# Kernel tuning notes

Measured on AMD Instinct MI355X. Metric: run time of the kernel, lower is better.

The kernel has to match this reference:

```python
import jax, jax.numpy as jnp
import numpy as np

HID = 5120
H_DEV = 16          # 128 heads / 8 devices
NOPE = 128
ROPE = 64
VDIM = 128
QH = NOPE + ROPE    # 192
Q_LORA = 1536
KV_LORA = 512
EPS = 1e-6
SCALE_DEV = 1.0 / 8.0
ROPE_BASE = 10000.0


def rmsnorm(x, w):
    var = jnp.mean(x * x, axis=-1, keepdims=True)
    return x * jax.lax.rsqrt(var + EPS) * w


def apply_rope(x, pos):
    # DeepSeek-V2: interleaved->blocked reorder, then rotate-half RoPE.
    d = x.shape[-1]
    x = jnp.concatenate([x[..., 0::2], x[..., 1::2]], axis=-1)
    inv = 1.0 / (ROPE_BASE ** (jnp.arange(0, d, 2, dtype=jnp.float32) / d))  # [d/2]
    ang = pos[:, None, :, None].astype(jnp.float32) * inv                     # [b,1,s,d/2]
    cos = jnp.concatenate([jnp.cos(ang), jnp.cos(ang)], axis=-1)
    sin = jnp.concatenate([jnp.sin(ang), jnp.sin(ang)], axis=-1)
    x1, x2 = x[..., : d // 2], x[..., d // 2:]
    return x * cos + jnp.concatenate([-x2, x1], axis=-1) * sin


def setup_inputs() -> dict:
    key = jax.random.key(0)
    ks = jax.random.split(key, 16)
    b, s, past = 1, 2048, 2048
    w = lambda k, shape: (jax.random.normal(k, shape, jnp.float32) * 0.02)
    return {
        "hidden_states": jax.random.normal(ks[0], (b, s, HID), jnp.float32),
        "position_ids": jnp.arange(b * s, dtype=jnp.int32).reshape(b, s),
        "attention_mask": jnp.zeros((b, 1, s, past + s), jnp.float32),
        "past_k": jax.random.normal(ks[1], (b, H_DEV, past, QH), jnp.float32),
        "past_v": jax.random.normal(ks[2], (b, H_DEV, past, VDIM), jnp.float32),
        "w_in_ln": jnp.ones((HID,), jnp.float32),
        "w_qa": w(ks[3], (Q_LORA, HID)),
        "w_qa_ln": jnp.ones((Q_LORA,), jnp.float32),
        "w_qb": w(ks[4], (H_DEV * QH, Q_LORA)),
        "w_kva": w(ks[5], (KV_LORA + ROPE, HID)),
        "w_kva_ln": jnp.ones((KV_LORA,), jnp.float32),
        "w_kvb": w(ks[6], (H_DEV * (NOPE + VDIM), KV_LORA)),
        "w_o": w(ks[7], (HID, H_DEV * VDIM)),
    }


def reference(hidden_states, position_ids, attention_mask, past_k, past_v,
              w_in_ln, w_qa, w_qa_ln, w_qb, w_kva, w_kva_ln, w_kvb, w_o):
    b, s, _ = hidden_states.shape
    residual = hidden_states * SCALE_DEV
    x = rmsnorm(hidden_states, w_in_ln)

    # MLA query: low-rank down, RMSNorm, up to per-device heads
    q = rmsnorm(x @ w_qa.T, w_qa_ln) @ w_qb.T                       # [b,s,H*QH]
    q = q.reshape(b, s, H_DEV, QH).transpose(0, 2, 1, 3)            # [b,H,s,QH]
    q_nope, q_pe = q[..., :NOPE], q[..., NOPE:]

    # MLA key/value: joint compressed kv + shared rope key
    ckv = x @ w_kva.T                                                # [b,s,KV_LORA+ROPE]
    c_kv, k_pe = ckv[..., :KV_LORA], ckv[..., KV_LORA:]
    kv = rmsnorm(c_kv, w_kva_ln) @ w_kvb.T                           # [b,s,H*(NOPE+V)]
    kv = kv.reshape(b, s, H_DEV, NOPE + VDIM).transpose(0, 2, 1, 3)  # [b,H,s,NOPE+V]
    k_nope, v = kv[..., :NOPE], kv[..., NOPE:]
    k_pe = k_pe.reshape(b, 1, s, ROPE)

    q_pe = apply_rope(q_pe, position_ids)
    k_pe = apply_rope(k_pe, position_ids)

    q = jnp.concatenate([q_nope, q_pe], axis=-1)                     # [b,H,s,QH]
    k = jnp.concatenate([k_nope, jnp.broadcast_to(k_pe, (b, H_DEV, s, ROPE))], axis=-1)

    # KV-cache concat -> present kv
    k = jnp.concatenate([past_k, k], axis=2)                         # [b,H,s_kv,QH]
    v = jnp.concatenate([past_v, v], axis=2)                         # [b,H,s_kv,V]

    scores = jnp.einsum('bhqd,bhkd->bhqk', q, k) * (QH ** -0.5) + attention_mask
    attn = jax.nn.softmax(scores, axis=-1)
    ctx = jnp.einsum('bhqk,bhkd->bhqd', attn, v)                     # [b,H,s,V]
    ctx = ctx.transpose(0, 2, 1, 3).reshape(b, s, H_DEV * VDIM)

    out = residual + ctx @ w_o.T
    return out.astype(jnp.float32), k.astype(jnp.float32), v.astype(jnp.float32)
```

## Files before the change

### kernel.cpp

```cpp
#include <hip/hip_runtime.h>
#include <cstdint>

typedef unsigned short ushort_t;
typedef __attribute__((ext_vector_type(8))) short short8;
typedef __attribute__((ext_vector_type(4))) float floatx4;

#define HID    5120
#define NHEAD  16
#define NOPE   128
#define ROPE_D 64
#define VDIM   128
#define QHD    192
#define QLORA  1536
#define KVLORA 512
#define SEQ    2048
#define PAST   2048
#define TOTK   4096
#define EPS_RMS 1e-6f
#define SCALE_DEV 0.125f
#define LOG2E 1.4426950408889634f
#define ATT_SCALE 0.07216878364870322f
#define LOG2_10000 13.287712379549449f

__device__ __forceinline__ float bf2f(ushort_t u) {
  unsigned int x = ((unsigned int)u) << 16;
  return __builtin_bit_cast(float, x);
}
__device__ __forceinline__ ushort_t f2bf(float f) {
  unsigned int u = __builtin_bit_cast(unsigned int, f);
  unsigned int r = u + 0x7fffu + ((u >> 16) & 1u);
  return (ushort_t)(r >> 16);
}
__device__ __forceinline__ void unpack8(uint4 c, float* f) {
  const ushort_t* p = (const ushort_t*)&c;
#pragma unroll
  for (int i = 0; i < 8; ++i) f[i] = bf2f(p[i]);
}
__device__ __forceinline__ uint4 pack8(const float* f) {
  uint4 c;
  ushort_t* p = (ushort_t*)&c;
#pragma unroll
  for (int i = 0; i < 8; ++i) p[i] = f2bf(f[i]);
  return c;
}

__global__ void cvt_kernel(const float* __restrict__ src, ushort_t* __restrict__ dst)
{
  long i = ((long)blockIdx.x * 256 + threadIdx.x) * 8;
  float f[8];
  *(float4*)(f)     = *(const float4*)(src + i);
  *(float4*)(f + 4) = *(const float4*)(src + i + 4);
  *(uint4*)(dst + i) = pack8(f);
}

#define GLDT 40
__global__ __launch_bounds__(256, 2) void gemm_bt(
    const ushort_t* __restrict__ A, const ushort_t* __restrict__ B,
    ushort_t* __restrict__ Cb, float* __restrict__ Cf,
    const float* __restrict__ resid, float resid_scale,
    int M, int N, int K)
{
  __shared__ __align__(16) ushort_t As[128 * GLDT];
  __shared__ __align__(16) ushort_t Bs[128 * GLDT];
  int t = threadIdx.x;
  int lane = t & 63, wave = t >> 6;
  int wm = wave >> 1, wn = wave & 1;
  int lrow = lane & 15, quad = lane >> 4;
  long bm = (long)blockIdx.y * 128;
  long bn = (long)blockIdx.x * 128;

  int r0 = t >> 2, cc = t & 3;
  int r1 = r0 + 64;
  const ushort_t* a0 = A + (bm + r0) * (long)K + cc * 8;
  const ushort_t* a1 = A + (bm + r1) * (long)K + cc * 8;
  long nb0 = bn + r0; if (nb0 > N - 1) nb0 = N - 1;
  long nb1 = bn + r1; if (nb1 > N - 1) nb1 = N - 1;
  const ushort_t* b0 = B + nb0 * (long)K + cc * 8;
  const ushort_t* b1 = B + nb1 * (long)K + cc * 8;

  floatx4 acc[4][4];
#pragma unroll
  for (int i = 0; i < 4; ++i)
#pragma unroll
    for (int j = 0; j < 4; ++j) acc[i][j] = (floatx4)0.f;

  uint4 pa0 = *(const uint4*)a0;
  uint4 pa1 = *(const uint4*)a1;
  uint4 pb0 = *(const uint4*)b0;
  uint4 pb1 = *(const uint4*)b1;

  int nk = K >> 5;
  for (int kt = 0; kt < nk; ++kt) {
    *(uint4*)&As[r0 * GLDT + cc * 8] = pa0;
    *(uint4*)&As[r1 * GLDT + cc * 8] = pa1;
    *(uint4*)&Bs[r0 * GLDT + cc * 8] = pb0;
    *(uint4*)&Bs[r1 * GLDT + cc * 8] = pb1;
    __syncthreads();
    if (kt + 1 < nk) {
      int off = (kt + 1) << 5;
      pa0 = *(const uint4*)(a0 + off);
      pa1 = *(const uint4*)(a1 + off);
      pb0 = *(const uint4*)(b0 + off);
      pb1 = *(const uint4*)(b1 + off);
    }
    short8 af[4], bfr[4];
#pragma unroll
    for (int mt = 0; mt < 4; ++mt)
      af[mt] = *(const short8*)&As[(wm * 64 + mt * 16 + lrow) * GLDT + quad * 8];
#pragma unroll
    for (int nt = 0; nt < 4; ++nt)
      bfr[nt] = *(const short8*)&Bs[(wn * 64 + nt * 16 + lrow) * GLDT + quad * 8];
#pragma unroll
    for (int mt = 0; mt < 4; ++mt)
#pragma unroll
      for (int nt = 0; nt < 4; ++nt)
        acc[mt][nt] = __builtin_amdgcn_mfma_f32_16x16x32_bf16(af[mt], bfr[nt], acc[mt][nt], 0, 0, 0);
    __syncthreads();
  }

#pragma unroll
  for (int mt = 0; mt < 4; ++mt) {
    long grow = bm + wm * 64 + mt * 16 + quad * 4;
#pragma unroll
    for (int nt = 0; nt < 4; ++nt) {
      long gcol = bn + wn * 64 + nt * 16 + lrow;
      if (gcol < N) {
#pragma unroll
        for (int r2 = 0; r2 < 4; ++r2) {
          long row = grow + r2;
          float v = acc[mt][nt][r2];
          if (Cf) {
            if (resid) v += resid_scale * resid[row * (long)N + gcol];
            Cf[row * (long)N + gcol] = v;
          } else {
            Cb[row * (long)N + gcol] = f2bf(v);
          }
        }
      }
    }
  }
}

__global__ void rms_in_kernel(const float* __restrict__ x,
                              const float* __restrict__ w,
                              ushort_t* __restrict__ out)
{
  int row = blockIdx.x, t = threadIdx.x;
  const float* xr = x + (long)row * HID + t * 16;
  float v[16];
#pragma unroll
  for (int i = 0; i < 4; ++i) *(float4*)(v + i * 4) = *(const float4*)(xr + i * 4);
  float ss = 0.f;
#pragma unroll
  for (int i = 0; i < 16; ++i) ss += v[i] * v[i];
#pragma unroll
  for (int o = 1; o < 64; o <<= 1) ss += __shfl_xor(ss, o);
  __shared__ float red[5];
  if ((t & 63) == 0) red[t >> 6] = ss;
  __syncthreads();
  float tot = red[0] + red[1] + red[2] + red[3] + red[4];
  float sc = rsqrtf(tot / (float)HID + EPS_RMS);
  float wv[16];
#pragma unroll
  for (int i = 0; i < 4; ++i) *(float4*)(wv + i * 4) = *(const float4*)(w + t * 16 + i * 4);
#pragma unroll
  for (int i = 0; i < 16; ++i) v[i] *= sc * wv[i];
  ushort_t* o = out + (long)row * HID + t * 16;
  *(uint4*)o       = pack8(v);
  *(uint4*)(o + 8) = pack8(v + 8);
}

__global__ void rms_qa_kernel(const ushort_t* __restrict__ x,
                              const float* __restrict__ w,
                              ushort_t* __restrict__ out)
{
  int row = blockIdx.x, t = threadIdx.x;
  const ushort_t* xr = x + (long)row * QLORA;
  float v[8];
  unpack8(*(const uint4*)(xr + t * 8), v);
  float ss = 0.f;
#pragma unroll
  for (int i = 0; i < 8; ++i) ss += v[i] * v[i];
#pragma unroll
  for (int o = 1; o < 64; o <<= 1) ss += __shfl_xor(ss, o);
  __shared__ float red[3];
  if ((t & 63) == 0) red[t >> 6] = ss;
  __syncthreads();
  float tot = red[0] + red[1] + red[2];
  float sc = rsqrtf(tot / (float)QLORA + EPS_RMS);
  float wv[8];
  *(float4*)(wv)     = *(const float4*)(w + t * 8);
  *(float4*)(wv + 4) = *(const float4*)(w + t * 8 + 4);
#pragma unroll
  for (int i = 0; i < 8; ++i) v[i] *= sc * wv[i];
  *(uint4*)(out + (long)row * QLORA + t * 8) = pack8(v);
}

__global__ void rms_ckv_rope(const ushort_t* __restrict__ ckv_raw,
                             const float* __restrict__ w,
                             const int* __restrict__ pos_ids,
                             ushort_t* __restrict__ ckv_n,
                             ushort_t* __restrict__ kpe,
                             float* __restrict__ k_out)
{
  int row = blockIdx.x, t = threadIdx.x;
  const ushort_t* xr = ckv_raw + (long)row * 576;
  float v[8];
  unpack8(*(const uint4*)(xr + t * 8), v);
  float ss = 0.f;
#pragma unroll
  for (int i = 0; i < 8; ++i) ss += v[i] * v[i];
#pragma unroll
  for (int o = 1; o < 64; o <<= 1) ss += __shfl_xor(ss, o);
  float sc = rsqrtf(ss / (float)KVLORA + EPS_RMS);
  float wv[8];
  *(float4*)(wv)     = *(const float4*)(w + t * 8);
  *(float4*)(wv + 4) = *(const float4*)(w + t * 8 + 4);
  float ov[8];
#pragma unroll
  for (int i = 0; i < 8; ++i) ov[i] = v[i] * sc * wv[i];
  *(uint4*)(ckv_n + (long)row * KVLORA + t * 8) = pack8(ov);

  if (t < 32) {
    float e  = bf2f(xr[512 + 2 * t]);
    float od = bf2f(xr[512 + 2 * t + 1]);
    float p = (float)pos_ids[row];
    float inv = __builtin_exp2f(-((float)t / 32.f) * LOG2_10000);
    float ang = p * inv, sn, cs;
    sincosf(ang, &sn, &cs);
    float r1 = e * cs - od * sn;
    float r2 = od * cs + e * sn;
    kpe[(long)row * 64 + t]      = f2bf(r1);
    kpe[(long)row * 64 + 32 + t] = f2bf(r2);
#pragma unroll
    for (int h = 0; h < NHEAD; ++h) {
      float* kr = k_out + ((long)h * TOTK + PAST + row) * QHD + NOPE;
      kr[t] = r1;
      kr[32 + t] = r2;
    }
  }
}

__global__ void qpost_kernel(const ushort_t* __restrict__ q_raw,
                             const int* __restrict__ pos_ids,
                             ushort_t* __restrict__ q_bf)
{
  int row = blockIdx.x, t = threadIdx.x;
  const ushort_t* qr = q_raw + (long)row * 3072;
  ushort_t* qo = q_bf + (long)row * 3072;
  {
    int hh = t >> 4, c = t & 15;
    float v[8];
    unpack8(*(const uint4*)(qr + hh * QHD + c * 8), v);
#pragma unroll
    for (int i = 0; i < 8; ++i) v[i] *= ATT_SCALE;
    *(uint4*)(qo + hh * QHD + c * 8) = pack8(v);
  }
  float p = (float)pos_ids[row];
#pragma unroll
  for (int it = 0; it < 2; ++it) {
    int slot = t + it * 256;
    int hh = slot >> 5, i = slot & 31;
    float e  = bf2f(qr[hh * QHD + NOPE + 2 * i]);
    float od = bf2f(qr[hh * QHD + NOPE + 2 * i + 1]);
    float inv = __builtin_exp2f(-((float)i / 32.f) * LOG2_10000);
    float ang = p * inv, sn, cs;
    sincosf(ang, &sn, &cs);
    qo[hh * QHD + NOPE + i]      = f2bf((e * cs - od * sn) * ATT_SCALE);
    qo[hh * QHD + NOPE + 32 + i] = f2bf((od * cs + e * sn) * ATT_SCALE);
  }
}

__global__ void kvpost_kernel(const ushort_t* __restrict__ kv_raw,
                              float* __restrict__ k_out,
                              float* __restrict__ v_out)
{
  int row = blockIdx.x, t = threadIdx.x;
  const ushort_t* kr = kv_raw + (long)row * 4096;
#pragma unroll
  for (int it = 0; it < 2; ++it) {
    int c = t + it * 256;
    int hh = c >> 5, cc = c & 31;
    float v[8];
    unpack8(*(const uint4*)(kr + c * 8), v);
    float* dst;
    if (cc < 16) dst = k_out + ((long)hh * TOTK + PAST + row) * QHD + cc * 8;
    else         dst = v_out + ((long)hh * TOTK + PAST + row) * VDIM + (cc - 16) * 8;
    floatx4 f0 = {v[0], v[1], v[2], v[3]};
    floatx4 f1 = {v[4], v[5], v[6], v[7]};
    *(floatx4*)dst = f0;
    *(floatx4*)(dst + 4) = f1;
  }
}

__global__ void past_kernel(const float* __restrict__ past_k,
                            const float* __restrict__ past_v,
                            float* __restrict__ k_out,
                            float* __restrict__ v_out)
{
  long c = (long)blockIdx.x * 256 + threadIdx.x;
  if (c < 1572864) {
    float4 v = *(const float4*)(past_k + c * 4);
    long hh = c / 98304, rem = c % 98304;
    long s = rem / 48, cc = rem % 48;
    *(float4*)(k_out + (hh * (long)TOTK + s) * QHD + cc * 4) = v;
  } else {
    long c2 = c - 1572864;
    float4 v = *(const float4*)(past_v + c2 * 4);
    long hh = c2 / 65536, rem = c2 % 65536;
    long s = rem / 32, cc = rem % 32;
    *(float4*)(v_out + (hh * (long)TOTK + s) * VDIM + cc * 4) = v;
  }
}

__global__ void buildK_kernel(const float* __restrict__ past_k,
                              const ushort_t* __restrict__ kv_raw,
                              const ushort_t* __restrict__ kpe,
                              ushort_t* __restrict__ Kc)
{
  long g = (long)blockIdx.x * 256 + threadIdx.x;
  int ko = (int)(g & 63);
  long r = g >> 6;
  int cc = (int)(r % 24);
  long r2 = r / 24;
  int kt = (int)(r2 & 63);
  int hh = (int)(r2 >> 6);
  int key = kt * 64 + ko;
  uint4 val;
  if (key < PAST) {
    const float* src = past_k + ((long)hh * PAST + key) * QHD + cc * 8;
    float f[8];
    *(float4*)(f)     = *(const float4*)src;
    *(float4*)(f + 4) = *(const float4*)(src + 4);
    val = pack8(f);
  } else {
    int s = key - PAST;
    int d0 = cc * 8;
    if (d0 < NOPE) val = *(const uint4*)(kv_raw + (long)s * 4096 + hh * 256 + d0);
    else           val = *(const uint4*)(kpe + (long)s * 64 + (d0 - NOPE));
  }
  *(uint4*)(Kc + g * 8) = val;
}

__global__ void buildV_kernel(const float* __restrict__ past_v,
                              const ushort_t* __restrict__ kv_raw,
                              ushort_t* __restrict__ Vc)
{
  long tid = (long)blockIdx.x * 256 + threadIdx.x;
  int vd = (int)(tid & 127);
  long r = tid >> 7;
  int kchunk = (int)(r & 7);
  long r2 = r >> 3;
  int kt = (int)(r2 & 63);
  int hh = (int)(r2 >> 6);
  int key0 = kt * 64 + kchunk * 8;
  __align__(16) ushort_t tmp[8];
  if (key0 < PAST) {
#pragma unroll
    for (int j = 0; j < 8; ++j)
      tmp[j] = f2bf(past_v[((long)hh * PAST + key0 + j) * VDIM + vd]);
  } else {
    int s = key0 - PAST;
#pragma unroll
    for (int j = 0; j < 8; ++j)
      tmp[j] = kv_raw[(long)(s + j) * 4096 + hh * 256 + NOPE + vd];
  }
  *(uint4*)(Vc + ((((long)hh * 64 + kt) * 128 + vd) * 9 + kchunk) * 8) = *(uint4*)tmp;
}

__global__ __launch_bounds__(256, 2) void attn_kernel(
    const ushort_t* __restrict__ qb,
    const ushort_t* __restrict__ Kc,
    const ushort_t* __restrict__ Vc,
    const float* __restrict__ attn_mask,
    ushort_t* __restrict__ ctx)
{
  __shared__ __align__(16) ushort_t KtL[1536 * 8];
  __shared__ __align__(16) ushort_t VtL[1152 * 8];
  __shared__ __align__(16) ushort_t Pl[4 * 16 * 72];

  int t = threadIdx.x, lane = t & 63, wave = t >> 6;
  int lrow = lane & 15, quad = lane >> 4;
  int h = blockIdx.y;
  int q0 = blockIdx.x * 64;
  int qrow_a = q0 + wave * 16 + lrow;
  int qrow_c = q0 + wave * 16 + quad * 4;

  short8 aq[6];
  const ushort_t* qp = qb + ((long)qrow_a * 16 + h) * QHD + quad * 8;
#pragma unroll
  for (int kc = 0; kc < 6; ++kc) aq[kc] = *(const short8*)(qp + kc * 32);

  float m_r[4], l_r[4];
  floatx4 cacc[8];
#pragma unroll
  for (int r = 0; r < 4; ++r) { m_r[r] = -1e30f; l_r[r] = 0.f; }
#pragma unroll
  for (int v = 0; v < 8; ++v) cacc[v] = (floatx4)0.f;

  const ushort_t* Kbase = Kc + (long)h * 64 * 1536 * 8;
  const ushort_t* Vbase = Vc + (long)h * 64 * 1152 * 8;

  for (int kt2 = 0; kt2 < 64; ++kt2) {
    const ushort_t* ks = Kbase + (long)kt2 * 1536 * 8;
#pragma unroll
    for (int i = 0; i < 6; ++i) {
      int s = i * 256 + t;
      *(uint4*)&KtL[s * 8] = *(const uint4*)(ks + (long)s * 8);
    }
    const ushort_t* vs = Vbase + (long)kt2 * 1152 * 8;
#pragma unroll
    for (int i = 0; i < 5; ++i) {
      int s = i * 256 + t;
      if (s < 1152) *(uint4*)&VtL[s * 8] = *(const uint4*)(vs + (long)s * 8);
    }
    __syncthreads();

    floatx4 sacc[4];
#pragma unroll
    for (int nt = 0; nt < 4; ++nt) sacc[nt] = (floatx4)0.f;
#pragma unroll
    for (int kc = 0; kc < 6; ++kc) {
#pragma unroll
      for (int nt = 0; nt < 4; ++nt) {
        short8 bk = *(const short8*)&KtL[(((kc * 4 + quad) * 64) + nt * 16 + lrow) * 8];
        sacc[nt] = __builtin_amdgcn_mfma_f32_16x16x32_bf16(aq[kc], bk, sacc[nt], 0, 0, 0);
      }
    }

    int kbase = kt2 * 64;
    float sv[4][4];
#pragma unroll
    for (int nt = 0; nt < 4; ++nt)
#pragma unroll
      for (int r = 0; r < 4; ++r)
        sv[nt][r] = sacc[nt][r] +
                    attn_mask[(long)(qrow_c + r) * TOTK + kbase + nt * 16 + lrow];

    float alpha[4];
#pragma unroll
    for (int r = 0; r < 4; ++r) {
      float mx = fmaxf(fmaxf(sv[0][r], sv[1][r]), fmaxf(sv[2][r], sv[3][r]));
      mx = fmaxf(mx, __shfl_xor(mx, 1));
      mx = fmaxf(mx, __shfl_xor(mx, 2));
      mx = fmaxf(mx, __shfl_xor(mx, 4));
      mx = fmaxf(mx, __shfl_xor(mx, 8));
      float mn = fmaxf(m_r[r], mx);
      alpha[r] = __builtin_exp2f((m_r[r] - mn) * LOG2E);
      m_r[r] = mn;
      float rs = 0.f;
#pragma unroll
      for (int nt = 0; nt < 4; ++nt) {
        float p = __builtin_exp2f((sv[nt][r] - mn) * LOG2E);
        sv[nt][r] = p;
        rs += p;
      }
      rs += __shfl_xor(rs, 1);
      rs += __shfl_xor(rs, 2);
      rs += __shfl_xor(rs, 4);
      rs += __shfl_xor(rs, 8);
      l_r[r] = l_r[r] * alpha[r] + rs;
    }
#pragma unroll
    for (int v = 0; v < 8; ++v) {
      floatx4 c = cacc[v];
      c[0] *= alpha[0]; c[1] *= alpha[1]; c[2] *= alpha[2]; c[3] *= alpha[3];
      cacc[v] = c;
    }

    ushort_t* pw = &Pl[wave * 16 * 72];
#pragma unroll
    for (int nt = 0; nt < 4; ++nt)
#pragma unroll
      for (int r = 0; r < 4; ++r)
        pw[(quad * 4 + r) * 72 + nt * 16 + lrow] = f2bf(sv[nt][r]);
    __syncthreads();

    const ushort_t* pr = &Pl[wave * 16 * 72];
    short8 ap[2];
#pragma unroll
    for (int kc = 0; kc < 2; ++kc)
      ap[kc] = *(const short8*)(pr + lrow * 72 + kc * 32 + quad * 8);
#pragma unroll
    for (int kc = 0; kc < 2; ++kc) {
#pragma unroll
      for (int v = 0; v < 8; ++v) {
        short8 bv = *(const short8*)&VtL[(((v * 16 + lrow) * 9) + kc * 4 + quad) * 8];
        cacc[v] = __builtin_amdgcn_mfma_f32_16x16x32_bf16(ap[kc], bv, cacc[v], 0, 0, 0);
      }
    }
    __syncthreads();
  }

#pragma unroll
  for (int v = 0; v < 8; ++v)
#pragma unroll
    for (int r = 0; r < 4; ++r) {
      float o = cacc[v][r] / l_r[r];
      ctx[(long)(qrow_c + r) * 2048 + h * 128 + v * 16 + lrow] = f2bf(o);
    }
}

extern "C" void kernel_launch(void* const* d_in, const int* in_sizes, int n_in,
                              void* d_out, int out_size, void* d_ws, size_t ws_size,
                              hipStream_t stream)
{
  const float* hidden   = (const float*)d_in[0];
  const int*   pos      = (const int*)d_in[1];
  const float* mask     = (const float*)d_in[2];
  const float* past_k   = (const float*)d_in[3];
  const float* past_v   = (const float*)d_in[4];
  const float* w_in_ln  = (const float*)d_in[5];
  const float* w_qa     = (const float*)d_in[6];
  const float* w_qa_ln  = (const float*)d_in[7];
  const float* w_qb     = (const float*)d_in[8];
  const float* w_kva    = (const float*)d_in[9];
  const float* w_kva_ln = (const float*)d_in[10];
  const float* w_kvb    = (const float*)d_in[11];
  const float* w_o      = (const float*)d_in[12];

  float* out0  = (float*)d_out;
  float* k_out = out0 + 10485760;
  float* v_out = k_out + 12582912;

  char* ws = (char*)d_ws;
  ushort_t* x_bf   = (ushort_t*)(ws + 0);
  ushort_t* q_raw  = x_bf;
  ushort_t* kv_raw = x_bf;
  ushort_t* qa_raw = (ushort_t*)(ws + 20971520);
  ushort_t* qa_n   = (ushort_t*)(ws + 27262976);
  ushort_t* ckv_raw= (ushort_t*)(ws + 33554432);
  ushort_t* ckv_n  = (ushort_t*)(ws + 35913728);
  ushort_t* kpe    = (ushort_t*)(ws + 38010880);
  ushort_t* q_bf   = (ushort_t*)(ws + 38273024);
  ushort_t* Kc     = (ushort_t*)(ws + 50855936);
  ushort_t* Vc     = (ushort_t*)(ws + 76021760);
  ushort_t* ctx    = (ushort_t*)(ws + 94896128);

  ushort_t* wqa_bf  = Kc;
  ushort_t* wkva_bf = (ushort_t*)(ws + 50855936 + 15728640);
  ushort_t* wqb_bf  = Vc;
  ushort_t* wkvb_bf = (ushort_t*)(ws + 76021760 + 9437184);
  ushort_t* wo_bf   = Kc;

  cvt_kernel<<<dim3(3840), dim3(256), 0, stream>>>(w_qa, wqa_bf);
  cvt_kernel<<<dim3(1440), dim3(256), 0, stream>>>(w_kva, wkva_bf);
  cvt_kernel<<<dim3(2304), dim3(256), 0, stream>>>(w_qb, wqb_bf);
  cvt_kernel<<<dim3(1024), dim3(256), 0, stream>>>(w_kvb, wkvb_bf);

  rms_in_kernel<<<dim3(2048), dim3(320), 0, stream>>>(hidden, w_in_ln, x_bf);

  gemm_bt<<<dim3(12, 16), dim3(256), 0, stream>>>(x_bf, wqa_bf, qa_raw, (float*)nullptr,
                                                  (const float*)nullptr, 0.f, 2048, 1536, 5120);
  gemm_bt<<<dim3(5, 16), dim3(256), 0, stream>>>(x_bf, wkva_bf, ckv_raw, (float*)nullptr,
                                                 (const float*)nullptr, 0.f, 2048, 576, 5120);

  rms_qa_kernel<<<dim3(2048), dim3(192), 0, stream>>>(qa_raw, w_qa_ln, qa_n);
  rms_ckv_rope<<<dim3(2048), dim3(64), 0, stream>>>(ckv_raw, w_kva_ln, pos, ckv_n, kpe, k_out);

  gemm_bt<<<dim3(24, 16), dim3(256), 0, stream>>>(qa_n, wqb_bf, q_raw, (float*)nullptr,
                                                  (const float*)nullptr, 0.f, 2048, 3072, 1536);
  qpost_kernel<<<dim3(2048), dim3(256), 0, stream>>>(q_raw, pos, q_bf);

  gemm_bt<<<dim3(32, 16), dim3(256), 0, stream>>>(ckv_n, wkvb_bf, kv_raw, (float*)nullptr,
                                                  (const float*)nullptr, 0.f, 2048, 4096, 512);
  kvpost_kernel<<<dim3(2048), dim3(256), 0, stream>>>(kv_raw, k_out, v_out);
  past_kernel<<<dim3(10240), dim3(256), 0, stream>>>(past_k, past_v, k_out, v_out);

  buildK_kernel<<<dim3(6144), dim3(256), 0, stream>>>(past_k, kv_raw, kpe, Kc);
  buildV_kernel<<<dim3(4096), dim3(256), 0, stream>>>(past_v, kv_raw, Vc);

  attn_kernel<<<dim3(32, 16), dim3(256), 0, stream>>>(q_bf, Kc, Vc, mask, ctx);

  cvt_kernel<<<dim3(5120), dim3(256), 0, stream>>>(w_o, wo_bf);

  gemm_bt<<<dim3(40, 16), dim3(256), 0, stream>>>(ctx, wo_bf, (ushort_t*)nullptr, out0,
                                                  hidden, SCALE_DEV, 2048, 5120, 2048);
}
```

Baseline: 957.4 us.

## Load GEMM and attention tiles directly into LDS and remap attention blocks per XCD

```diff
diff --git a/kernel.cpp b/kernel.cpp
--- a/kernel.cpp
+++ b/kernel.cpp
@@ -44,6 +44,12 @@
   return c;
 }
 
+__device__ __forceinline__ void gload16(const ushort_t* g, ushort_t* l) {
+  __builtin_amdgcn_global_load_lds(
+      (const __attribute__((address_space(1))) unsigned int*)g,
+      (__attribute__((address_space(3))) unsigned int*)l, 16, 0, 0);
+}
+
 __global__ void cvt_kernel(const float* __restrict__ src, ushort_t* __restrict__ dst)
 {
   long i = ((long)blockIdx.x * 256 + threadIdx.x) * 8;
@@ -53,15 +59,14 @@
   *(uint4*)(dst + i) = pack8(f);
 }
 
-#define GLDT 40
 __global__ __launch_bounds__(256, 2) void gemm_bt(
     const ushort_t* __restrict__ A, const ushort_t* __restrict__ B,
     ushort_t* __restrict__ Cb, float* __restrict__ Cf,
     const float* __restrict__ resid, float resid_scale,
     int M, int N, int K)
 {
-  __shared__ __align__(16) ushort_t As[128 * GLDT];
-  __shared__ __align__(16) ushort_t Bs[128 * GLDT];
+  __shared__ __align__(16) ushort_t As[128 * 32];
+  __shared__ __align__(16) ushort_t Bs[128 * 32];
   int t = threadIdx.x;
   int lane = t & 63, wave = t >> 6;
   int wm = wave >> 1, wn = wave & 1;
@@ -69,47 +74,41 @@
   long bm = (long)blockIdx.y * 128;
   long bn = (long)blockIdx.x * 128;
 
-  int r0 = t >> 2, cc = t & 3;
+  int r0 = t >> 2, c8 = (t & 3) * 8;
   int r1 = r0 + 64;
-  const ushort_t* a0 = A + (bm + r0) * (long)K + cc * 8;
-  const ushort_t* a1 = A + (bm + r1) * (long)K + cc * 8;
+  const ushort_t* a0 = A + (bm + r0) * (long)K + c8;
+  const ushort_t* a1 = A + (bm + r1) * (long)K + c8;
   long nb0 = bn + r0; if (nb0 > N - 1) nb0 = N - 1;
   long nb1 = bn + r1; if (nb1 > N - 1) nb1 = N - 1;
-  const ushort_t* b0 = B + nb0 * (long)K + cc * 8;
-  const ushort_t* b1 = B + nb1 * (long)K + cc * 8;
+  const ushort_t* b0 = B + nb0 * (long)K + c8;
+  const ushort_t* b1 = B + nb1 * (long)K + c8;
+  ushort_t* dA0 = &As[(wave * 64) * 8];
+  ushort_t* dA1 = &As[(256 + wave * 64) * 8];
+  ushort_t* dB0 = &Bs[(wave * 64) * 8];
+  ushort_t* dB1 = &Bs[(256 + wave * 64) * 8];
 
   floatx4 acc[4][4];
 #pragma unroll
   for (int i = 0; i < 4; ++i)
 #pragma unroll
     for (int j = 0; j < 4; ++j) acc[i][j] = (floatx4)0.f;
-
-  uint4 pa0 = *(const uint4*)a0;
-  uint4 pa1 = *(const uint4*)a1;
-  uint4 pb0 = *(const uint4*)b0;
-  uint4 pb1 = *(const uint4*)b1;
 
   int nk = K >> 5;
   for (int kt = 0; kt < nk; ++kt) {
-    *(uint4*)&As[r0 * GLDT + cc * 8] = pa0;
-    *(uint4*)&As[r1 * GLDT + cc * 8] = pa1;
-    *(uint4*)&Bs[r0 * GLDT + cc * 8] = pb0;
-    *(uint4*)&Bs[r1 * GLDT + cc * 8] = pb1;
+    long ko = (long)kt * 32;
+    gload16(a0 + ko, dA0);
+    gload16(a1 + ko, dA1);
+    gload16(b0 + ko, dB0);
+    gload16(b1 + ko, dB1);
     __syncthreads();
-    if (kt + 1 < nk) {
-      int off = (kt + 1) << 5;
-      pa0 = *(const uint4*)(a0 + off);
-      pa1 = *(const uint4*)(a1 + off);
-      pb0 = *(const uint4*)(b0 + off);
-      pb1 = *(const uint4*)(b1 + off);
-    }
+
     short8 af[4], bfr[4];
 #pragma unroll
     for (int mt = 0; mt < 4; ++mt)
-      af[mt] = *(const short8*)&As[(wm * 64 + mt * 16 + lrow) * GLDT + quad * 8];
+      af[mt] = *(const short8*)&As[(wm * 64 + mt * 16 + lrow) * 32 + quad * 8];
 #pragma unroll
     for (int nt = 0; nt < 4; ++nt)
-      bfr[nt] = *(const short8*)&Bs[(wn * 64 + nt * 16 + lrow) * GLDT + quad * 8];
+      bfr[nt] = *(const short8*)&Bs[(wn * 64 + nt * 16 + lrow) * 32 + quad * 8];
 #pragma unroll
     for (int mt = 0; mt < 4; ++mt)
 #pragma unroll
@@ -368,7 +367,7 @@
   *(uint4*)(Vc + ((((long)hh * 64 + kt) * 128 + vd) * 9 + kchunk) * 8) = *(uint4*)tmp;
 }
 
-__global__ __launch_bounds__(256, 2) void attn_kernel(
+__global__ __launch_bounds__(256, 3) void attn_kernel(
     const ushort_t* __restrict__ qb,
     const ushort_t* __restrict__ Kc,
     const ushort_t* __restrict__ Vc,
@@ -381,8 +380,10 @@
 
   int t = threadIdx.x, lane = t & 63, wave = t >> 6;
   int lrow = lane & 15, quad = lane >> 4;
-  int h = blockIdx.y;
-  int q0 = blockIdx.x * 64;
+  int lb = blockIdx.y * 32 + blockIdx.x;
+  int xcd = lb & 7, j = lb >> 3;
+  int h = xcd + 8 * (j >> 5);
+  int q0 = (j & 31) * 64;
   int qrow_a = q0 + wave * 16 + lrow;
   int qrow_c = q0 + wave * 16 + quad * 4;
 
@@ -405,14 +406,14 @@
     const ushort_t* ks = Kbase + (long)kt2 * 1536 * 8;
 #pragma unroll
     for (int i = 0; i < 6; ++i) {
-      int s = i * 256 + t;
-      *(uint4*)&KtL[s * 8] = *(const uint4*)(ks + (long)s * 8);
+      int c = i * 4 + wave;
+      gload16(ks + ((long)c * 64 + lane) * 8, &KtL[c * 64 * 8]);
     }
     const ushort_t* vs = Vbase + (long)kt2 * 1152 * 8;
 #pragma unroll
     for (int i = 0; i < 5; ++i) {
-      int s = i * 256 + t;
-      if (s < 1152) *(uint4*)&VtL[s * 8] = *(const uint4*)(vs + (long)s * 8);
+      int c = i * 4 + wave;
+      if (c < 18) gload16(vs + ((long)c * 64 + lane) * 8, &VtL[c * 64 * 8]);
     }
     __syncthreads();
 
```

New measurement: 1.043 ms. 1.09x slower.

## Split attention KV range into three sections with a combine kernel

Applied to the files above, without the earlier changes.

```diff
diff --git a/kernel.cpp b/kernel.cpp
--- a/kernel.cpp
+++ b/kernel.cpp
@@ -368,12 +368,13 @@
   *(uint4*)(Vc + ((((long)hh * 64 + kt) * 128 + vd) * 9 + kchunk) * 8) = *(uint4*)tmp;
 }
 
-__global__ __launch_bounds__(256, 2) void attn_kernel(
+__global__ __launch_bounds__(256, 3) void attn_kernel(
     const ushort_t* __restrict__ qb,
     const ushort_t* __restrict__ Kc,
     const ushort_t* __restrict__ Vc,
     const float* __restrict__ attn_mask,
-    ushort_t* __restrict__ ctx)
+    ushort_t* __restrict__ opart,
+    float* __restrict__ ml)
 {
   __shared__ __align__(16) ushort_t KtL[1536 * 8];
   __shared__ __align__(16) ushort_t VtL[1152 * 8];
@@ -381,8 +382,14 @@
 
   int t = threadIdx.x, lane = t & 63, wave = t >> 6;
   int lrow = lane & 15, quad = lane >> 4;
-  int h = blockIdx.y;
-  int q0 = blockIdx.x * 64;
+  int lb = blockIdx.x;
+  int xcd = lb & 7, j = lb >> 3;
+  int h = xcd + 8 * (j / 96);
+  int rem = j % 96;
+  int sec = rem >> 5;
+  int q0 = (rem & 31) * 64;
+  int kt_beg = (sec == 0) ? 0 : (sec == 1 ? 22 : 43);
+  int kt_end = (sec == 0) ? 22 : (sec == 1 ? 43 : 64);
   int qrow_a = q0 + wave * 16 + lrow;
   int qrow_c = q0 + wave * 16 + quad * 4;
 
@@ -401,7 +408,7 @@
   const ushort_t* Kbase = Kc + (long)h * 64 * 1536 * 8;
   const ushort_t* Vbase = Vc + (long)h * 64 * 1152 * 8;
 
-  for (int kt2 = 0; kt2 < 64; ++kt2) {
+  for (int kt2 = kt_beg; kt2 < kt_end; ++kt2) {
     const ushort_t* ks = Kbase + (long)kt2 * 1536 * 8;
 #pragma unroll
     for (int i = 0; i < 6; ++i) {
@@ -419,6 +426,7 @@
     floatx4 sacc[4];
 #pragma unroll
     for (int nt = 0; nt < 4; ++nt) sacc[nt] = (floatx4)0.f;
+    __builtin_amdgcn_s_setprio(1);
 #pragma unroll
     for (int kc = 0; kc < 6; ++kc) {
 #pragma unroll
@@ -427,6 +435,7 @@
         sacc[nt] = __builtin_amdgcn_mfma_f32_16x16x32_bf16(aq[kc], bk, sacc[nt], 0, 0, 0);
       }
     }
+    __builtin_amdgcn_s_setprio(0);
 
     int kbase = kt2 * 64;
     float sv[4][4];
@@ -474,13 +483,13 @@
 #pragma unroll
       for (int r = 0; r < 4; ++r)
         pw[(quad * 4 + r) * 72 + nt * 16 + lrow] = f2bf(sv[nt][r]);
-    __syncthreads();
 
     const ushort_t* pr = &Pl[wave * 16 * 72];
     short8 ap[2];
 #pragma unroll
     for (int kc = 0; kc < 2; ++kc)
       ap[kc] = *(const short8*)(pr + lrow * 72 + kc * 32 + quad * 8);
+    __builtin_amdgcn_s_setprio(1);
 #pragma unroll
     for (int kc = 0; kc < 2; ++kc) {
 #pragma unroll
@@ -489,16 +498,61 @@
         cacc[v] = __builtin_amdgcn_mfma_f32_16x16x32_bf16(ap[kc], bv, cacc[v], 0, 0, 0);
       }
     }
+    __builtin_amdgcn_s_setprio(0);
     __syncthreads();
   }
 
+  long obase = (long)(sec * 16 + h) * 2048 + qrow_c;
 #pragma unroll
   for (int v = 0; v < 8; ++v)
 #pragma unroll
+    for (int r = 0; r < 4; ++r)
+      opart[(obase + r) * 128 + v * 16 + lrow] = f2bf(cacc[v][r]);
+  if (lrow == 0) {
+#pragma unroll
     for (int r = 0; r < 4; ++r) {
-      float o = cacc[v][r] / l_r[r];
-      ctx[(long)(qrow_c + r) * 2048 + h * 128 + v * 16 + lrow] = f2bf(o);
-    }
+      float* mp = ml + (obase + r) * 2;
+      mp[0] = m_r[r];
+      mp[1] = l_r[r];
+    }
+  }
+}
+
+__global__ void combine_kernel(const ushort_t* __restrict__ opart,
+                               const float* __restrict__ ml,
+                               ushort_t* __restrict__ ctx)
+{
+  int t = threadIdx.x;
+  int gr = blockIdx.x * 16 + (t >> 4);
+  int h = gr >> 11, qrow = gr & 2047;
+  int dc = (t & 15) * 8;
+  float m[3], l[3];
+#pragma unroll
+  for (int s = 0; s < 3; ++s) {
+    const float* p = ml + ((long)(s * 16 + h) * 2048 + qrow) * 2;
+    m[s] = p[0]; l[s] = p[1];
+  }
+  float M = fmaxf(fmaxf(m[0], m[1]), m[2]);
+  float aa[3], L = 0.f;
+#pragma unroll
+  for (int s = 0; s < 3; ++s) {
+    aa[s] = __builtin_exp2f((m[s] - M) * LOG2E);
+    L += aa[s] * l[s];
+  }
+  float inv = 1.f / L;
+  float acc[8] = {0.f, 0.f, 0.f, 0.f, 0.f, 0.f, 0.f, 0.f};
+#pragma unroll
+  for (int s = 0; s < 3; ++s) {
+    uint4 c = *(const uint4*)(opart + ((long)(s * 16 + h) * 2048 + qrow) * 128 + dc);
+    float f[8];
+    unpack8(c, f);
+#pragma unroll
+    for (int i = 0; i < 8; ++i) acc[i] += aa[s] * f[i];
+  }
+  float outv[8];
+#pragma unroll
+  for (int i = 0; i < 8; ++i) outv[i] = acc[i] * inv;
+  *(uint4*)(ctx + (long)qrow * 2048 + h * 128 + dc) = pack8(outv);
 }
 
 extern "C" void kernel_launch(void* const* d_in, const int* in_sizes, int n_in,
@@ -537,6 +591,9 @@
   ushort_t* Vc     = (ushort_t*)(ws + 76021760);
   ushort_t* ctx    = (ushort_t*)(ws + 94896128);
 
+  ushort_t* opart  = (ushort_t*)(ws + 0);
+  float*    mlbuf  = (float*)(ws + 25165824);
+
   ushort_t* wqa_bf  = Kc;
   ushort_t* wkva_bf = (ushort_t*)(ws + 50855936 + 15728640);
   ushort_t* wqb_bf  = Vc;
@@ -570,7 +627,8 @@
   buildK_kernel<<<dim3(6144), dim3(256), 0, stream>>>(past_k, kv_raw, kpe, Kc);
   buildV_kernel<<<dim3(4096), dim3(256), 0, stream>>>(past_v, kv_raw, Vc);
 
-  attn_kernel<<<dim3(32, 16), dim3(256), 0, stream>>>(q_bf, Kc, Vc, mask, ctx);
+  attn_kernel<<<dim3(1536), dim3(256), 0, stream>>>(q_bf, Kc, Vc, mask, opart, mlbuf);
+  combine_kernel<<<dim3(2048), dim3(256), 0, stream>>>(opart, mlbuf, ctx);
 
   cvt_kernel<<<dim3(5120), dim3(256), 0, stream>>>(w_o, wo_bf);
 
```

Result: faster. 898.3 us (-6.2%).
